# Kernel optimization log

Measured on AMD Instinct MI355X. Metric: run time of the kernel, lower is better.

## Reference

```python
import jax, jax.numpy as jnp
import numpy as np

HS, FF, NH = 1024, 4096, 16
HD = HS // NH
EPS = 1e-5

def _ln(x, g, b):
    m = jnp.mean(x, axis=-1, keepdims=True)
    v = jnp.mean((x - m) ** 2, axis=-1, keepdims=True)
    return (x - m) * jax.lax.rsqrt(v + EPS) * g + b

def setup_inputs() -> dict:
    key = jax.random.key(0)
    ks = jax.random.split(key, 12)
    s = 1.0 / np.sqrt(HS)
    si = 1.0 / np.sqrt(FF)
    d = {
        "hidden_states": jax.random.normal(ks[0], (2, 2048, HS), dtype=jnp.float32),
        "attention_mask": jnp.zeros((2, 1, 1, 2048), dtype=jnp.float32),
        "Wq": jax.random.uniform(ks[1], (HS, HS), minval=-s, maxval=s),
        "bq": jnp.zeros((HS,), jnp.float32),
        "Wk": jax.random.uniform(ks[2], (HS, HS), minval=-s, maxval=s),
        "bk": jnp.zeros((HS,), jnp.float32),
        "Wv": jax.random.uniform(ks[3], (HS, HS), minval=-s, maxval=s),
        "bv": jnp.zeros((HS,), jnp.float32),
        "Wo": jax.random.uniform(ks[4], (HS, HS), minval=-s, maxval=s),
        "bo": jnp.zeros((HS,), jnp.float32),
        "W1": jax.random.uniform(ks[5], (HS, FF), minval=-s, maxval=s),
        "b1": jnp.zeros((FF,), jnp.float32),
        "W2": jax.random.uniform(ks[6], (FF, HS), minval=-si, maxval=si),
        "b2": jnp.zeros((HS,), jnp.float32),
        "ln1_g": jnp.ones((HS,), jnp.float32),
        "ln1_b": jnp.zeros((HS,), jnp.float32),
        "ln2_g": jnp.ones((HS,), jnp.float32),
        "ln2_b": jnp.zeros((HS,), jnp.float32),
    }
    return d

def reference(hidden_states, attention_mask, Wq, bq, Wk, bk, Wv, bv, Wo, bo,
              W1, b1, W2, b2, ln1_g, ln1_b, ln2_g, ln2_b):
    bs, S, _ = hidden_states.shape
    x = hidden_states
    # self-attention (dropout is identity in eval)
    q = (x @ Wq + bq).reshape(bs, S, NH, HD).transpose(0, 2, 1, 3)
    k = (x @ Wk + bk).reshape(bs, S, NH, HD).transpose(0, 2, 1, 3)
    v = (x @ Wv + bv).reshape(bs, S, NH, HD).transpose(0, 2, 1, 3)
    scores = jnp.einsum("bhqd,bhkd->bhqk", q, k) / np.sqrt(HD) + attention_mask
    probs = jax.nn.softmax(scores, axis=-1)
    attn = jnp.einsum("bhqk,bhkd->bhqd", probs, v)
    attn = attn.transpose(0, 2, 1, 3).reshape(bs, S, HS)
    mha = attn @ Wo + bo
    h = _ln(x + mha, ln1_g, ln1_b)
    # FFN
    ff = jax.nn.relu(h @ W1 + b1) @ W2 + b2
    return _ln(h + ff, ln2_g, ln2_b)
```

## Files before the change

kernel.cpp:

```cpp
#include <hip/hip_runtime.h>
#include <hip/hip_bf16.h>

#define HS   1024
#define FF   4096
#define NH   16
#define HD   64
#define SEQ  2048
#define BSZ  2
#define MROWS (BSZ * SEQ)
#define EPS  1e-5f
#define QKV_STRIDE (3 * HS)

typedef float f32x4  __attribute__((ext_vector_type(4)));
typedef short bf16x8 __attribute__((ext_vector_type(8)));

__device__ __forceinline__ unsigned short f2bf(float x) {
  unsigned int u = __float_as_uint(x);
  u += 0x7fffu + ((u >> 16) & 1u);
  return (unsigned short)(u >> 16);
}

__device__ __forceinline__ unsigned int pkbf(float a, float b) {
  union { __hip_bfloat162 h; unsigned int u; } x;
  x.h = __float22bfloat162_rn(float2{a, b});
  return x.u;
}

__device__ __forceinline__ void async16(const ushort* g, ushort* lds) {
  __builtin_amdgcn_global_load_lds(
      (const __attribute__((address_space(1))) unsigned int*)g,
      (__attribute__((address_space(3))) unsigned int*)lds, 16, 0, 0);
}

template <int TBM, int TBN, bool RELU, bool OUT_BF16, bool PARTIAL>
__global__ __launch_bounds__(256) void gemm_bf16_kernel(
    const ushort* __restrict__ A, const ushort* __restrict__ Bt,
    const float* __restrict__ bias, void* __restrict__ Cout,
    int M, int N, int K, int kLen, size_t zstride)
{
  constexpr int MI = TBM / 32;
  constexpr int NJ = TBN / 32;
  __shared__ ushort As[TBM * 64];
  __shared__ ushort Bs[TBN * 64];

  const int tid = threadIdx.x;
  const int wv = tid >> 6, ln = tid & 63;
  const int bn = blockIdx.x, bm = blockIdx.y;

  const int lr = ln & 15;
  const int lg = ln >> 4;
  const int mrow_base = (wv >> 1) * (TBM / 2);
  const int ncol_base = (wv & 1) * (TBN / 2);

  f32x4 acc[MI][NJ];
#pragma unroll
  for (int i = 0; i < MI; ++i)
#pragma unroll
    for (int j = 0; j < NJ; ++j) acc[i][j] = (f32x4){0.f, 0.f, 0.f, 0.f};

  const int rr = ln >> 3, cc = ln & 7;
  const int kBeg = blockIdx.z * kLen, kEnd = kBeg + kLen;

  for (int k0 = kBeg; k0 < kEnd; k0 += 64) {
    __syncthreads();
#pragma unroll
    for (int t = 0; t < TBM / 32; ++t) {
      const int R = wv * (TBM / 4) + t * 8 + rr;
      const int c = cc ^ (R & 7);
      async16(A + (size_t)(bm * TBM + R) * K + k0 + c * 8,
              &As[(size_t)(wv * (TBM / 4) + t * 8) * 64]);
    }
#pragma unroll
    for (int t = 0; t < TBN / 32; ++t) {
      const int R = wv * (TBN / 4) + t * 8 + rr;
      const int c = cc ^ (R & 7);
      async16(Bt + (size_t)(bn * TBN + R) * K + k0 + c * 8,
              &Bs[(size_t)(wv * (TBN / 4) + t * 8) * 64]);
    }
    __syncthreads();

#pragma unroll
    for (int s = 0; s < 2; ++s) {
      bf16x8 a[MI], b[NJ];
#pragma unroll
      for (int i = 0; i < MI; ++i) {
        const int m = mrow_base + i * 16 + lr;
        a[i] = *(const bf16x8*)&As[(size_t)m * 64 + (((s * 4 + lg) ^ (m & 7)) * 8)];
      }
#pragma unroll
      for (int j = 0; j < NJ; ++j) {
        const int n = ncol_base + j * 16 + lr;
        b[j] = *(const bf16x8*)&Bs[(size_t)n * 64 + (((s * 4 + lg) ^ (n & 7)) * 8)];
      }
#pragma unroll
      for (int i = 0; i < MI; ++i)
#pragma unroll
        for (int j = 0; j < NJ; ++j)
          acc[i][j] = __builtin_amdgcn_mfma_f32_16x16x32_bf16(a[i], b[j], acc[i][j], 0, 0, 0);
    }
  }

  const int gm0 = bm * TBM + mrow_base;
  const int gn0 = bn * TBN + ncol_base;

  if (PARTIAL) {
    float* Cp = (float*)Cout + (size_t)blockIdx.z * zstride;
#pragma unroll
    for (int i = 0; i < MI; ++i)
#pragma unroll
      for (int r = 0; r < 4; ++r) {
        const size_t row = (size_t)(gm0 + i * 16 + lg * 4 + r);
#pragma unroll
        for (int j = 0; j < NJ; ++j)
          Cp[row * N + gn0 + j * 16 + lr] = acc[i][j][r];
      }
  } else {
    float bs4[NJ];
#pragma unroll
    for (int j = 0; j < NJ; ++j) bs4[j] = bias[gn0 + j * 16 + lr];
    float* Cf = (float*)Cout;
    ushort* Cb = (ushort*)Cout;
#pragma unroll
    for (int i = 0; i < MI; ++i) {
#pragma unroll
      for (int r = 0; r < 4; ++r) {
        const size_t row = (size_t)(gm0 + i * 16 + lg * 4 + r);
#pragma unroll
        for (int j = 0; j < NJ; ++j) {
          float val = acc[i][j][r] + bs4[j];
          if (RELU) val = fmaxf(val, 0.f);
          const size_t idx = row * N + gn0 + j * 16 + lr;
          if (OUT_BF16) Cb[idx] = f2bf(val);
          else          Cf[idx] = val;
        }
      }
    }
  }
}

__device__ __forceinline__ void transpose_tile(
    const float* __restrict__ W, ushort* __restrict__ Wt,
    int K, int N, int n0, int k0, int tid, ushort (*T)[72])
{
#pragma unroll
  for (int t = 0; t < 4; ++t) {
    const int r = t * 16 + (tid >> 4);
    const int c = (tid & 15) * 4;
    const float4 w = *(const float4*)&W[(size_t)(k0 + r) * N + n0 + c];
    T[c + 0][r] = f2bf(w.x); T[c + 1][r] = f2bf(w.y);
    T[c + 2][r] = f2bf(w.z); T[c + 3][r] = f2bf(w.w);
  }
  __syncthreads();
#pragma unroll
  for (int t = 0; t < 4; ++t) {
    const int n = t * 16 + (tid >> 4);
    const int kc = (tid & 15) * 4;
    ushort4 o;
    o.x = T[n][kc]; o.y = T[n][kc + 1]; o.z = T[n][kc + 2]; o.w = T[n][kc + 3];
    *(ushort4*)&Wt[(size_t)(n0 + n) * K + k0 + kc] = o;
  }
}

__global__ __launch_bounds__(256) void prep_kernel(
    const float* __restrict__ Wq, const float* __restrict__ Wk,
    const float* __restrict__ Wv, const float* __restrict__ Wo,
    const float* __restrict__ W1, const float* __restrict__ W2,
    const float* __restrict__ bq, const float* __restrict__ bk,
    const float* __restrict__ bv, const float* __restrict__ x,
    ushort* __restrict__ Wqkvt, ushort* __restrict__ Wot,
    ushort* __restrict__ W1t, ushort* __restrict__ W2t,
    float* __restrict__ bqkv, ushort* __restrict__ xb)
{
  __shared__ ushort T[64][72];
  const int b = blockIdx.x, tid = threadIdx.x;
  const size_t M1 = 1024 * 1024;
  if (b < 1024) {
    const int w = b >> 8, l = b & 255;
    const int n0 = (l & 15) * 64, k0 = (l >> 4) * 64;
    const float* src = (w == 0) ? Wq : (w == 1) ? Wk : (w == 2) ? Wv : Wo;
    ushort* dst = (w < 3) ? (Wqkvt + (size_t)w * M1) : Wot;
    transpose_tile(src, dst, HS, HS, n0, k0, tid, T);
  } else if (b < 2048) {
    const int l = b - 1024;
    transpose_tile(W1, W1t, HS, FF, (l & 63) * 64, (l >> 6) * 64, tid, T);
  } else if (b < 3072) {
    const int l = b - 2048;
    transpose_tile(W2, W2t, FF, HS, (l & 15) * 64, (l >> 4) * 64, tid, T);
  } else if (b < 5120) {
    const size_t base = (size_t)(b - 3072) * 2048 + tid * 8;
    const float4 v0 = *(const float4*)&x[base];
    const float4 v1 = *(const float4*)&x[base + 4];
    ushort4 o0, o1;
    o0.x = f2bf(v0.x); o0.y = f2bf(v0.y); o0.z = f2bf(v0.z); o0.w = f2bf(v0.w);
    o1.x = f2bf(v1.x); o1.y = f2bf(v1.y); o1.z = f2bf(v1.z); o1.w = f2bf(v1.w);
    *(ushort4*)&xb[base] = o0;
    *(ushort4*)&xb[base + 4] = o1;
  } else {
#pragma unroll
    for (int t = 0; t < 12; ++t) {
      const int i = t * 256 + tid;
      bqkv[i] = (i < HS) ? bq[i] : (i < 2 * HS) ? bk[i - HS] : bv[i - 2 * HS];
    }
  }
}

__global__ __launch_bounds__(256) void vtrans_kernel(
    const ushort* __restrict__ vb, ushort* __restrict__ VTg, int stride)
{
  __shared__ ushort T[64][68];
  const int tid = threadIdx.x;
  const int s0 = blockIdx.x * 64;
  const int bh = blockIdx.y;
  const int b = bh >> 4, h = bh & 15;
#pragma unroll
  for (int t = 0; t < 4; ++t) {
    const int rr = t * 16 + (tid >> 4);
    const int c4 = (tid & 15) * 4;
    const ushort4 w = *(const ushort4*)&vb[(size_t)(b * SEQ + s0 + rr) * stride + h * 64 + c4];
    T[c4 + 0][rr] = w.x; T[c4 + 1][rr] = w.y;
    T[c4 + 2][rr] = w.z; T[c4 + 3][rr] = w.w;
  }
  __syncthreads();
#pragma unroll
  for (int t = 0; t < 4; ++t) {
    const int d = t * 16 + (tid >> 4);
    const int k4 = (tid & 15) * 4;
    ushort4 o;
    o.x = T[d][k4]; o.y = T[d][k4 + 1]; o.z = T[d][k4 + 2]; o.w = T[d][k4 + 3];
    *(ushort4*)&VTg[((size_t)bh * 64 + d) * SEQ + s0 + k4] = o;
  }
}

__global__ __launch_bounds__(256, 2) void attention_mfma_kernel(
    const ushort* __restrict__ Qb, const ushort* __restrict__ Kb,
    const ushort* __restrict__ VTg, const float* __restrict__ mask,
    ushort* __restrict__ O)
{
  __shared__ ushort smem[36864];
  float* mL = (float*)(smem + 32768);

  const int tid = threadIdx.x;
  const int wv = tid >> 6, ln = tid & 63;
  const int c = ln & 15, g = ln >> 4;
  const int qt = blockIdx.x, hh = blockIdx.y, b = blockIdx.z;
  const int bh = b * NH + hh;
  const size_t row0 = (size_t)b * SEQ + (size_t)qt * 128;
  const int ch = hh * HD;
  const int wq0 = wv * 32;

  bf16x8 qf[2][2];
#pragma unroll
  for (int nt = 0; nt < 2; ++nt)
#pragma unroll
    for (int s = 0; s < 2; ++s)
      qf[nt][s] = *(const bf16x8*)&Qb[(row0 + wq0 + nt * 16 + c) * QKV_STRIDE + ch + s * 32 + g * 8];

  const float* mrow = mask + (size_t)b * SEQ;
#pragma unroll
  for (int t = 0; t < 2; ++t)
    async16((const ushort*)(mrow + t * 1024 + wv * 256 + ln * 4),
            (ushort*)(mL + t * 1024 + wv * 256));

  const int rr = ln >> 3, cc = ln & 7;
  const int r4 = ln >> 4, sc = ln & 15;

  auto stage = [&](int kb, int bsel) {
    ushort* Ks  = smem + bsel * 16384;
    ushort* VTs = Ks + 8192;
    const size_t krow0 = (size_t)b * SEQ + (size_t)kb * 128;
#pragma unroll
    for (int t = 0; t < 4; ++t) {
      const int r = wv * 32 + t * 8 + rr;
      async16(Kb + (krow0 + r) * QKV_STRIDE + ch + ((cc ^ (r & 7)) * 8),
              &Ks[(size_t)(wv * 32 + t * 8) * 64]);
    }
#pragma unroll
    for (int t = 0; t < 4; ++t) {
      const int d = wv * 16 + t * 4 + r4;
      const int srcc = (sc & 8) | ((sc & 7) ^ (d & 7));
      async16(VTg + ((size_t)bh * 64 + d) * SEQ + kb * 128 + srcc * 8,
              &VTs[(size_t)(wv * 16 + t * 4) * 128]);
    }
  };

  f32x4 ao[4][2];
#pragma unroll
  for (int i = 0; i < 4; ++i) { ao[i][0] = (f32x4){0,0,0,0}; ao[i][1] = (f32x4){0,0,0,0}; }
  float l_r[2] = {0.f, 0.f};

  stage(0, 0);

  for (int kb = 0; kb < SEQ / 128; ++kb) {
    const int cur = kb & 1;
    __builtin_amdgcn_s_barrier();
    __builtin_amdgcn_sched_barrier(0);
    if (kb + 1 < SEQ / 128) {
      stage(kb + 1, cur ^ 1);
      asm volatile("s_waitcnt vmcnt(8)" ::: "memory");
    } else {
      asm volatile("s_waitcnt vmcnt(0)" ::: "memory");
    }
    __builtin_amdgcn_s_barrier();
    __builtin_amdgcn_sched_barrier(0);

    ushort* Ks  = smem + cur * 16384;
    ushort* VTs = Ks + 8192;

    f32x4 as_[8][2];
#pragma unroll
    for (int i = 0; i < 8; ++i) { as_[i][0] = (f32x4){0,0,0,0}; as_[i][1] = (f32x4){0,0,0,0}; }
    __builtin_amdgcn_s_setprio(1);
#pragma unroll
    for (int s = 0; s < 2; ++s) {
#pragma unroll
      for (int mt = 0; mt < 8; ++mt) {
        const int key = mt * 16 + c;
        const bf16x8 kf = *(const bf16x8*)&Ks[(size_t)key * 64 + (((s * 4 + g) ^ (key & 7)) * 8)];
#pragma unroll
        for (int nt = 0; nt < 2; ++nt)
          as_[mt][nt] = __builtin_amdgcn_mfma_f32_16x16x32_bf16(kf, qf[nt][s], as_[mt][nt], 0, 0, 0);
      }
    }
    __builtin_amdgcn_s_setprio(0);

#pragma unroll
    for (int mt = 0; mt < 8; ++mt) {
      const float4 mk = *(const float4*)&mL[kb * 128 + mt * 16 + g * 4];
      const float mka[4] = {mk.x, mk.y, mk.z, mk.w};
#pragma unroll
      for (int nt = 0; nt < 2; ++nt) {
#pragma unroll
        for (int r = 0; r < 4; ++r) {
          const float p = __expf(fminf(as_[mt][nt][r] * 0.125f + mka[r], 60.f));
          as_[mt][nt][r] = p;
          l_r[nt] += p;
        }
      }
    }

#pragma unroll
    for (int s = 0; s < 4; ++s) {
      bf16x8 pf[2];
#pragma unroll
      for (int nt = 0; nt < 2; ++nt) {
        const unsigned A0 = pkbf(as_[2 * s][nt][0], as_[2 * s][nt][1]);
        const unsigned A1 = pkbf(as_[2 * s][nt][2], as_[2 * s][nt][3]);
        const unsigned B0 = pkbf(as_[2 * s + 1][nt][0], as_[2 * s + 1][nt][1]);
        const unsigned B1 = pkbf(as_[2 * s + 1][nt][2], as_[2 * s + 1][nt][3]);
        auto x0 = __builtin_amdgcn_permlane32_swap(A0, B0, false, false);
        auto x1 = __builtin_amdgcn_permlane32_swap(A1, B1, false, false);
        auto y0 = __builtin_amdgcn_permlane16_swap(x0[0], x0[1], false, false);
        auto y1 = __builtin_amdgcn_permlane16_swap(x1[0], x1[1], false, false);
        union { unsigned w[4]; bf16x8 v; } u;
        u.w[0] = y0[0]; u.w[1] = y1[0]; u.w[2] = y0[1]; u.w[3] = y1[1];
        pf[nt] = u.v;
      }
      __builtin_amdgcn_s_setprio(1);
#pragma unroll
      for (int mt = 0; mt < 4; ++mt) {
        const int d = mt * 16 + c;
        const int k = s * 4 + g;
        const int vslot = (k & 8) | ((k & 7) ^ (d & 7));
        const bf16x8 vf = *(const bf16x8*)&VTs[(size_t)d * 128 + vslot * 8];
#pragma unroll
        for (int nt = 0; nt < 2; ++nt)
          ao[mt][nt] = __builtin_amdgcn_mfma_f32_16x16x32_bf16(vf, pf[nt], ao[mt][nt], 0, 0, 0);
      }
      __builtin_amdgcn_s_setprio(0);
    }
  }

#pragma unroll
  for (int nt = 0; nt < 2; ++nt) {
    l_r[nt] += __shfl_xor(l_r[nt], 16, 64);
    l_r[nt] += __shfl_xor(l_r[nt], 32, 64);
  }

  __syncthreads();
  ushort* OL = smem;
#pragma unroll
  for (int nt = 0; nt < 2; ++nt) {
    const float inv = 1.f / l_r[nt];
    const int q = wq0 + nt * 16 + c;
#pragma unroll
    for (int mt = 0; mt < 4; ++mt) {
      const int d = mt * 16 + g * 4;
      uint2 w;
      w.x = pkbf(ao[mt][nt][0] * inv, ao[mt][nt][1] * inv);
      w.y = pkbf(ao[mt][nt][2] * inv, ao[mt][nt][3] * inv);
      *(uint2*)&OL[q * 72 + d] = w;
    }
  }
  __syncthreads();
#pragma unroll
  for (int it = 0; it < 4; ++it) {
    const int unit = it * 256 + tid;
    const int q = unit >> 3, sg = unit & 7;
    const uint4 w = *(const uint4*)&OL[q * 72 + sg * 8];
    *(uint4*)&O[(row0 + q) * HS + ch + sg * 8] = w;
  }
}

template <bool EMIT16>
__global__ __launch_bounds__(256) void add_ln_red_kernel(
    const float* __restrict__ P0, const float* __restrict__ P1,
    const float* __restrict__ bias, const float* __restrict__ X,
    const float* __restrict__ g, const float* __restrict__ b,
    float* __restrict__ out, ushort* __restrict__ outb)
{
  const int row = blockIdx.x;
  const int tid = threadIdx.x;
  const size_t base = (size_t)row * HS + tid * 4;
  const float4 p0 = *(const float4*)&P0[base];
  const float4 p1 = *(const float4*)&P1[base];
  const float4 bi = *(const float4*)&bias[tid * 4];
  const float4 xv = *(const float4*)&X[base];
  float4 v;
  v.x = xv.x + p0.x + p1.x + bi.x;
  v.y = xv.y + p0.y + p1.y + bi.y;
  v.z = xv.z + p0.z + p1.z + bi.z;
  v.w = xv.w + p0.w + p1.w + bi.w;
  float s1 = v.x + v.y + v.z + v.w;
  float s2 = v.x * v.x + v.y * v.y + v.z * v.z + v.w * v.w;
#pragma unroll
  for (int off = 32; off > 0; off >>= 1) {
    s1 += __shfl_down(s1, off, 64);
    s2 += __shfl_down(s2, off, 64);
  }
  __shared__ float red[8];
  __shared__ float stat[2];
  const int wid = tid >> 6;
  if ((tid & 63) == 0) { red[wid] = s1; red[4 + wid] = s2; }
  __syncthreads();
  if (tid == 0) {
    const float t1 = red[0] + red[1] + red[2] + red[3];
    const float t2 = red[4] + red[5] + red[6] + red[7];
    const float mean = t1 * (1.f / HS);
    const float var = t2 * (1.f / HS) - mean * mean;
    stat[0] = mean;
    stat[1] = rsqrtf(var + EPS);
  }
  __syncthreads();
  const float mean = stat[0], rstd = stat[1];
  const float4 gv = *(const float4*)&g[tid * 4];
  const float4 bv = *(const float4*)&b[tid * 4];
  float4 r;
  r.x = (v.x - mean) * rstd * gv.x + bv.x;
  r.y = (v.y - mean) * rstd * gv.y + bv.y;
  r.z = (v.z - mean) * rstd * gv.z + bv.z;
  r.w = (v.w - mean) * rstd * gv.w + bv.w;
  *(float4*)&out[base] = r;
  if (EMIT16) {
    ushort4 o;
    o.x = f2bf(r.x); o.y = f2bf(r.y); o.z = f2bf(r.z); o.w = f2bf(r.w);
    *(ushort4*)&outb[base] = o;
  }
}

extern "C" void kernel_launch(void* const* d_in, const int* in_sizes, int n_in,
                              void* d_out, int out_size, void* d_ws, size_t ws_size,
                              hipStream_t stream)
{
  const float* x    = (const float*)d_in[0];
  const float* mask = (const float*)d_in[1];
  const float* Wq   = (const float*)d_in[2];  const float* bq  = (const float*)d_in[3];
  const float* Wk   = (const float*)d_in[4];  const float* bk  = (const float*)d_in[5];
  const float* Wv   = (const float*)d_in[6];  const float* bv  = (const float*)d_in[7];
  const float* Wo   = (const float*)d_in[8];  const float* bo  = (const float*)d_in[9];
  const float* W1   = (const float*)d_in[10]; const float* b1  = (const float*)d_in[11];
  const float* W2   = (const float*)d_in[12]; const float* b2  = (const float*)d_in[13];
  const float* g1   = (const float*)d_in[14]; const float* be1 = (const float*)d_in[15];
  const float* g2   = (const float*)d_in[16]; const float* be2 = (const float*)d_in[17];
  float* out = (float*)d_out;

  ushort* wsu = (ushort*)d_ws;
  const size_t M1 = 1024 * 1024;

  ushort* Wqkvt = wsu;
  ushort* Wot   = wsu + 3 * M1;
  ushort* W1t   = wsu + 4 * M1;
  ushort* W2t   = wsu + 8 * M1;
  float*  bqkv  = (float*)(wsu + 12 * M1);
  ushort* xb    = wsu + 13 * M1;
  ushort* qkvb  = wsu + 17 * M1;
  ushort* VTg   = wsu + 29 * M1;
  ushort* attnb = wsu + 33 * M1;
  float*  woP   = (float*)(wsu + 13 * M1);
  float*  h     = (float*)(wsu + 29 * M1);
  ushort* hb    = wsu + 37 * M1;
  ushort* ff1o  = wsu + 13 * M1;
  float*  ff2P0 = (float*)wsu;
  float*  ff2P1 = (float*)(wsu + 39 * M1);

  const dim3 blk(256);
  const size_t SLAB = (size_t)MROWS * HS;

  prep_kernel<<<dim3(5121), blk, 0, stream>>>(
      Wq, Wk, Wv, Wo, W1, W2, bq, bk, bv, x,
      Wqkvt, Wot, W1t, W2t, bqkv, xb);

  gemm_bf16_kernel<128, 128, false, true, false><<<dim3(24, 32), blk, 0, stream>>>(
      xb, Wqkvt, bqkv, qkvb, MROWS, 3 * HS, HS, HS, 0);

  vtrans_kernel<<<dim3(SEQ / 64, BSZ * NH), blk, 0, stream>>>(qkvb + 2 * HS, VTg, QKV_STRIDE);

  attention_mfma_kernel<<<dim3(SEQ / 128, NH, BSZ), blk, 0, stream>>>(
      qkvb, qkvb + HS, VTg, mask, attnb);

  gemm_bf16_kernel<64, 128, false, false, true><<<dim3(8, 64, 2), blk, 0, stream>>>(
      attnb, Wot, nullptr, woP, MROWS, HS, HS, HS / 2, SLAB);
  add_ln_red_kernel<true><<<dim3(MROWS), blk, 0, stream>>>(
      woP, woP + SLAB, bo, x, g1, be1, h, hb);

  gemm_bf16_kernel<128, 128, true, true, false><<<dim3(32, 32), blk, 0, stream>>>(
      hb, W1t, b1, ff1o, MROWS, FF, HS, HS, 0);
  gemm_bf16_kernel<128, 128, false, false, true><<<dim3(8, 32, 2), blk, 0, stream>>>(
      ff1o, W2t, nullptr, ff2P0, MROWS, HS, FF, FF / 2, (size_t)(ff2P1 - ff2P0));
  add_ln_red_kernel<false><<<dim3(MROWS), blk, 0, stream>>>(
      ff2P0, ff2P1, b2, h, g2, be2, out, nullptr);
}
```

Baseline: 383.6 us.

## Swizzle block order, use exp2 softmax, and drop split-K for Wo projection

Remaps GEMM and attention block indices so that consecutive blocks spread across XCDs for better L2 locality. Switches the softmax exponent to exp2 by premultiplying the mask with log2(e) in the prep kernel and folding the scale into a fused multiply-add. Replaces the split-K Wo GEMM that wrote fp32 partials with a single-pass GEMM that adds the bias and writes bf16, followed by a new add+LayerNorm kernel that reads the bf16 result. This cuts memory traffic and the reduction cost, at the price of some precision in the MHA output and fewer blocks in flight for the Wo GEMM.

```diff
diff --git a/kernel.cpp b/kernel.cpp
--- a/kernel.cpp
+++ b/kernel.cpp
@@ -14,10 +14,20 @@
 typedef float f32x4  __attribute__((ext_vector_type(4)));
 typedef short bf16x8 __attribute__((ext_vector_type(8)));
 
+#if __has_builtin(__builtin_amdgcn_exp2f)
+#define EXP2(x) __builtin_amdgcn_exp2f(x)
+#else
+#define EXP2(x) exp2f(x)
+#endif
+
 __device__ __forceinline__ unsigned short f2bf(float x) {
   unsigned int u = __float_as_uint(x);
   u += 0x7fffu + ((u >> 16) & 1u);
   return (unsigned short)(u >> 16);
+}
+
+__device__ __forceinline__ float bf2f(unsigned short u) {
+  return __uint_as_float((unsigned int)u << 16);
 }
 
 __device__ __forceinline__ unsigned int pkbf(float a, float b) {
@@ -45,7 +55,11 @@
 
   const int tid = threadIdx.x;
   const int wv = tid >> 6, ln = tid & 63;
-  const int bn = blockIdx.x, bm = blockIdx.y;
+
+  const unsigned nxy = gridDim.x * gridDim.y;
+  unsigned id = blockIdx.y * gridDim.x + blockIdx.x;
+  id = (id & 7) * (nxy >> 3) + (id >> 3);
+  const int bn = id % gridDim.x, bm = id / gridDim.x;
 
   const int lr = ln & 15;
   const int lg = ln >> 4;
@@ -167,9 +181,11 @@
     const float* __restrict__ W1, const float* __restrict__ W2,
     const float* __restrict__ bq, const float* __restrict__ bk,
     const float* __restrict__ bv, const float* __restrict__ x,
+    const float* __restrict__ mask,
     ushort* __restrict__ Wqkvt, ushort* __restrict__ Wot,
     ushort* __restrict__ W1t, ushort* __restrict__ W2t,
-    float* __restrict__ bqkv, ushort* __restrict__ xb)
+    float* __restrict__ bqkv, ushort* __restrict__ xb,
+    float* __restrict__ maskL2)
 {
   __shared__ ushort T[64][72];
   const int b = blockIdx.x, tid = threadIdx.x;
@@ -201,6 +217,11 @@
       const int i = t * 256 + tid;
       bqkv[i] = (i < HS) ? bq[i] : (i < 2 * HS) ? bk[i - HS] : bv[i - 2 * HS];
     }
+#pragma unroll
+    for (int t = 0; t < 16; ++t) {
+      const int i = t * 256 + tid;
+      maskL2[i] = mask[i] * 1.44269504f;
+    }
   }
 }
 
@@ -233,7 +254,7 @@
 
 __global__ __launch_bounds__(256, 2) void attention_mfma_kernel(
     const ushort* __restrict__ Qb, const ushort* __restrict__ Kb,
-    const ushort* __restrict__ VTg, const float* __restrict__ mask,
+    const ushort* __restrict__ VTg, const float* __restrict__ maskL2,
     ushort* __restrict__ O)
 {
   __shared__ ushort smem[36864];
@@ -242,7 +263,13 @@
   const int tid = threadIdx.x;
   const int wv = tid >> 6, ln = tid & 63;
   const int c = ln & 15, g = ln >> 4;
-  const int qt = blockIdx.x, hh = blockIdx.y, b = blockIdx.z;
+
+  const unsigned d0 = blockIdx.x + 16u * (blockIdx.y + 16u * blockIdx.z);
+  const unsigned w0 = (d0 & 7) * 64 + (d0 >> 3);
+  const int qt = w0 & 15;
+  const int hh = (w0 >> 4) & 15;
+  const int b  = w0 >> 8;
+
   const int bh = b * NH + hh;
   const size_t row0 = (size_t)b * SEQ + (size_t)qt * 128;
   const int ch = hh * HD;
@@ -255,7 +282,7 @@
     for (int s = 0; s < 2; ++s)
       qf[nt][s] = *(const bf16x8*)&Qb[(row0 + wq0 + nt * 16 + c) * QKV_STRIDE + ch + s * 32 + g * 8];
 
-  const float* mrow = mask + (size_t)b * SEQ;
+  const float* mrow = maskL2 + (size_t)b * SEQ;
 #pragma unroll
   for (int t = 0; t < 2; ++t)
     async16((const ushort*)(mrow + t * 1024 + wv * 256 + ln * 4),
@@ -331,7 +358,7 @@
       for (int nt = 0; nt < 2; ++nt) {
 #pragma unroll
         for (int r = 0; r < 4; ++r) {
-          const float p = __expf(fminf(as_[mt][nt][r] * 0.125f + mka[r], 60.f));
+          const float p = EXP2(fminf(fmaf(as_[mt][nt][r], 0.18033688f, mka[r]), 86.56f));
           as_[mt][nt][r] = p;
           l_r[nt] += p;
         }
@@ -457,6 +484,56 @@
   }
 }
 
+__global__ __launch_bounds__(256) void add_ln_bf16_kernel(
+    const ushort* __restrict__ Pb, const float* __restrict__ X,
+    const float* __restrict__ g, const float* __restrict__ b,
+    float* __restrict__ out, ushort* __restrict__ outb)
+{
+  const int row = blockIdx.x;
+  const int tid = threadIdx.x;
+  const size_t base = (size_t)row * HS + tid * 4;
+  const ushort4 pb = *(const ushort4*)&Pb[base];
+  const float4 xv = *(const float4*)&X[base];
+  float4 v;
+  v.x = xv.x + bf2f(pb.x);
+  v.y = xv.y + bf2f(pb.y);
+  v.z = xv.z + bf2f(pb.z);
+  v.w = xv.w + bf2f(pb.w);
+  float s1 = v.x + v.y + v.z + v.w;
+  float s2 = v.x * v.x + v.y * v.y + v.z * v.z + v.w * v.w;
+#pragma unroll
+  for (int off = 32; off > 0; off >>= 1) {
+    s1 += __shfl_down(s1, off, 64);
+    s2 += __shfl_down(s2, off, 64);
+  }
+  __shared__ float red[8];
+  __shared__ float stat[2];
+  const int wid = tid >> 6;
+  if ((tid & 63) == 0) { red[wid] = s1; red[4 + wid] = s2; }
+  __syncthreads();
+  if (tid == 0) {
+    const float t1 = red[0] + red[1] + red[2] + red[3];
+    const float t2 = red[4] + red[5] + red[6] + red[7];
+    const float mean = t1 * (1.f / HS);
+    const float var = t2 * (1.f / HS) - mean * mean;
+    stat[0] = mean;
+    stat[1] = rsqrtf(var + EPS);
+  }
+  __syncthreads();
+  const float mean = stat[0], rstd = stat[1];
+  const float4 gv = *(const float4*)&g[tid * 4];
+  const float4 bv = *(const float4*)&b[tid * 4];
+  float4 r;
+  r.x = (v.x - mean) * rstd * gv.x + bv.x;
+  r.y = (v.y - mean) * rstd * gv.y + bv.y;
+  r.z = (v.z - mean) * rstd * gv.z + bv.z;
+  r.w = (v.w - mean) * rstd * gv.w + bv.w;
+  *(float4*)&out[base] = r;
+  ushort4 o;
+  o.x = f2bf(r.x); o.y = f2bf(r.y); o.z = f2bf(r.z); o.w = f2bf(r.w);
+  *(ushort4*)&outb[base] = o;
+}
+
 extern "C" void kernel_launch(void* const* d_in, const int* in_sizes, int n_in,
                               void* d_out, int out_size, void* d_ws, size_t ws_size,
                               hipStream_t stream)
@@ -481,11 +558,12 @@
   ushort* W1t   = wsu + 4 * M1;
   ushort* W2t   = wsu + 8 * M1;
   float*  bqkv  = (float*)(wsu + 12 * M1);
+  float*  maskL2= (float*)(wsu + 12 * M1 + 8192);
   ushort* xb    = wsu + 13 * M1;
   ushort* qkvb  = wsu + 17 * M1;
   ushort* VTg   = wsu + 29 * M1;
   ushort* attnb = wsu + 33 * M1;
-  float*  woP   = (float*)(wsu + 13 * M1);
+  ushort* mhab  = wsu + 13 * M1;
   float*  h     = (float*)(wsu + 29 * M1);
   ushort* hb    = wsu + 37 * M1;
   ushort* ff1o  = wsu + 13 * M1;
@@ -493,11 +571,10 @@
   float*  ff2P1 = (float*)(wsu + 39 * M1);
 
   const dim3 blk(256);
-  const size_t SLAB = (size_t)MROWS * HS;
 
   prep_kernel<<<dim3(5121), blk, 0, stream>>>(
-      Wq, Wk, Wv, Wo, W1, W2, bq, bk, bv, x,
-      Wqkvt, Wot, W1t, W2t, bqkv, xb);
+      Wq, Wk, Wv, Wo, W1, W2, bq, bk, bv, x, mask,
+      Wqkvt, Wot, W1t, W2t, bqkv, xb, maskL2);
 
   gemm_bf16_kernel<128, 128, false, true, false><<<dim3(24, 32), blk, 0, stream>>>(
       xb, Wqkvt, bqkv, qkvb, MROWS, 3 * HS, HS, HS, 0);
@@ -505,12 +582,12 @@
   vtrans_kernel<<<dim3(SEQ / 64, BSZ * NH), blk, 0, stream>>>(qkvb + 2 * HS, VTg, QKV_STRIDE);
 
   attention_mfma_kernel<<<dim3(SEQ / 128, NH, BSZ), blk, 0, stream>>>(
-      qkvb, qkvb + HS, VTg, mask, attnb);
-
-  gemm_bf16_kernel<64, 128, false, false, true><<<dim3(8, 64, 2), blk, 0, stream>>>(
-      attnb, Wot, nullptr, woP, MROWS, HS, HS, HS / 2, SLAB);
-  add_ln_red_kernel<true><<<dim3(MROWS), blk, 0, stream>>>(
-      woP, woP + SLAB, bo, x, g1, be1, h, hb);
+      qkvb, qkvb + HS, VTg, maskL2, attnb);
+
+  gemm_bf16_kernel<64, 128, false, true, false><<<dim3(8, 64), blk, 0, stream>>>(
+      attnb, Wot, bo, mhab, MROWS, HS, HS, HS, 0);
+  add_ln_bf16_kernel<<<dim3(MROWS), blk, 0, stream>>>(
+      mhab, x, g1, be1, h, hb);
 
   gemm_bf16_kernel<128, 128, true, true, false><<<dim3(32, 32), blk, 0, stream>>>(
       hb, W1t, b1, ff1o, MROWS, FF, HS, HS, 0);
```

New measurement: 368.8 us. -3.9%, faster.
